# Optimization experiments

Hardware: AMD Instinct MI355X
Metric: run time of the kernel (lower is better)

The kernel has to match this reference:

```python
import jax, jax.numpy as jnp
import numpy as np

BATCH = 2048
OBS_DIM = 48
H0, H1, H2 = 512, 256, 128
ACT_DIM = 12
NUM_TEACHERS = 64


def setup_inputs() -> dict:
    key = jax.random.key(0)
    ks = jax.random.split(key, 10)
    s = lambda fan_in: 1.0 / np.sqrt(fan_in)
    return {
        "obs": jax.random.normal(ks[0], (BATCH, OBS_DIM), dtype=jnp.float32),
        "teacher_indices": jax.random.randint(ks[1], (BATCH,), 0, NUM_TEACHERS),
        "w0": jax.random.normal(ks[2], (NUM_TEACHERS, H0, OBS_DIM), dtype=jnp.float32) * s(OBS_DIM),
        "b0": jax.random.normal(ks[3], (NUM_TEACHERS, H0), dtype=jnp.float32) * s(OBS_DIM),
        "w2": jax.random.normal(ks[4], (NUM_TEACHERS, H1, H0), dtype=jnp.float32) * s(H0),
        "b2": jax.random.normal(ks[5], (NUM_TEACHERS, H1), dtype=jnp.float32) * s(H0),
        "w4": jax.random.normal(ks[6], (NUM_TEACHERS, H2, H1), dtype=jnp.float32) * s(H1),
        "b4": jax.random.normal(ks[7], (NUM_TEACHERS, H2), dtype=jnp.float32) * s(H1),
        "w6": jax.random.normal(ks[8], (NUM_TEACHERS, ACT_DIM, H2), dtype=jnp.float32) * s(H2),
        "b6": jax.random.normal(ks[9], (NUM_TEACHERS, ACT_DIM), dtype=jnp.float32) * s(H2),
    }


def reference(obs, teacher_indices, w0, b0, w2, b2, w4, b4, w6, b6):
    # Per-sample gather of full teacher layer weights, then batched GEMV.
    def layer(x, w, b):
        # x: [B, in]; w[idx]: [B, out, in]; b[idx]: [B, out]
        return jnp.einsum("boi,bi->bo", w[teacher_indices], x) + b[teacher_indices]

    x = jax.nn.elu(layer(obs, w0, b0))
    x = jax.nn.elu(layer(x, w2, b2))
    x = jax.nn.elu(layer(x, w4, b4))
    x = jnp.tanh(layer(x, w6, b6))
    return x
```

## Files before the change

kernel.cpp:

```cpp
#include <hip/hip_runtime.h>

#define BATCH 2048
#define NTEACH 64

typedef __attribute__((ext_vector_type(8))) short short8;
typedef __attribute__((ext_vector_type(4))) float f32x4;

__device__ __forceinline__ unsigned short f2bf(float f) {
    unsigned u = __float_as_uint(f);
    u += 0x7FFFu + ((u >> 16) & 1u);
    return (unsigned short)(u >> 16);
}

__device__ __forceinline__ short8 cvt8(float4 a, float4 b) {
    short8 r;
    r[0] = (short)f2bf(a.x); r[1] = (short)f2bf(a.y);
    r[2] = (short)f2bf(a.z); r[3] = (short)f2bf(a.w);
    r[4] = (short)f2bf(b.x); r[5] = (short)f2bf(b.y);
    r[6] = (short)f2bf(b.z); r[7] = (short)f2bf(b.w);
    return r;
}

__device__ __forceinline__ int2 scan_teacher(const int* __restrict__ tidx,
                                             int t, int* ord) {
    __shared__ int ws_[4];
    const int tid = threadIdx.x;
    const int lane = tid & 63;
    const int wid = tid >> 6;
    int base = 0;
    int my_lt = 0;
#pragma unroll
    for (int r = 0; r < 8; ++r) {
        int i = r * 256 + tid;
        int v = tidx[i];
        bool f = (v == t);
        my_lt += (v < t) ? 1 : 0;
        unsigned long long b = __ballot(f);
        if (lane == 0) ws_[wid] = __builtin_popcountll(b);
        int below = __builtin_popcountll(b & ((1ull << lane) - 1ull));
        __syncthreads();
        int w0 = ws_[0], w1 = ws_[1], w2 = ws_[2], w3 = ws_[3];
        if (ord && f) {
            int wbase = (wid > 0 ? w0 : 0) + (wid > 1 ? w1 : 0) + (wid > 2 ? w2 : 0);
            ord[base + wbase + below] = i;
        }
        base += w0 + w1 + w2 + w3;
        __syncthreads();
    }
    for (int off = 32; off; off >>= 1) my_lt += __shfl_down(my_lt, off);
    if (lane == 0) ws_[wid] = my_lt;
    __syncthreads();
    int start = ws_[0] + ws_[1] + ws_[2] + ws_[3];
    __syncthreads();
    return make_int2(start, base);
}

__global__ __launch_bounds__(256) void l0_kernel(const float* __restrict__ obs,
                                                 const int* __restrict__ tidx,
                                                 const float* __restrict__ w0,
                                                 const float* __restrict__ b0,
                                                 unsigned short* __restrict__ h0) {
    __shared__ int ord[BATCH];
    const int t = blockIdx.y;
    int2 sc = scan_teacher(tidx, t, ord);
    const int start = sc.x, count = sc.y;
    if (count == 0) return;
    const int lane = threadIdx.x & 63, wid = threadIdx.x >> 6;
    const int ln = lane & 15, kg = lane >> 4;
    const int nq = wid & 1, mq = wid >> 1;
    const int n0 = blockIdx.x * 32 + nq * 16;

    short8 bf[2];
    const float* wr = w0 + ((size_t)t * 512 + n0 + ln) * 48;
#pragma unroll
    for (int kt = 0; kt < 2; ++kt) {
        int kb = kt * 32 + kg * 8;
        short8 f8 = {0, 0, 0, 0, 0, 0, 0, 0};
        if (kb < 48) f8 = cvt8(*(const float4*)(wr + kb), *(const float4*)(wr + kb + 4));
        bf[kt] = f8;
    }
    const float bias = b0[(size_t)t * 512 + n0 + ln];

    for (int r0 = mq * 16; r0 < count; r0 += 32) {
        int lr = r0 + ln;
        const float* xr = obs + (size_t)ord[lr < count ? lr : 0] * 48;
        short8 af[2];
#pragma unroll
        for (int kt = 0; kt < 2; ++kt) {
            int kb = kt * 32 + kg * 8;
            short8 f8 = {0, 0, 0, 0, 0, 0, 0, 0};
            if (kb < 48) f8 = cvt8(*(const float4*)(xr + kb), *(const float4*)(xr + kb + 4));
            af[kt] = f8;
        }
        f32x4 acc = {0.f, 0.f, 0.f, 0.f};
        acc = __builtin_amdgcn_mfma_f32_16x16x32_bf16(af[0], bf[0], acc, 0, 0, 0);
        acc = __builtin_amdgcn_mfma_f32_16x16x32_bf16(af[1], bf[1], acc, 0, 0, 0);
#pragma unroll
        for (int j = 0; j < 4; ++j) {
            int row = r0 + kg * 4 + j;
            if (row < count) {
                float v = acc[j] + bias;
                v = v > 0.f ? v : expm1f(v);
                h0[(size_t)(start + row) * 512 + n0 + ln] = f2bf(v);
            }
        }
    }
}

__global__ __launch_bounds__(256) void l1_kernel(const unsigned short* __restrict__ h0,
                                                 const int* __restrict__ tidx,
                                                 const float* __restrict__ w2,
                                                 const float* __restrict__ b2,
                                                 unsigned short* __restrict__ h1) {
    __shared__ f32x4 red[2][64];
    const int t = blockIdx.y;
    int2 sc = scan_teacher(tidx, t, nullptr);
    const int start = sc.x, count = sc.y;
    if (count == 0) return;
    const int lane = threadIdx.x & 63, wid = threadIdx.x >> 6;
    const int ln = lane & 15, kg = lane >> 4;
    const int kq = wid & 1, nq = wid >> 1;
    const int n0 = blockIdx.x * 32 + nq * 16;
    const int kbase = kq * 256;

    short8 bf[8];
    const float* wr = w2 + ((size_t)t * 256 + n0 + ln) * 512 + kbase;
#pragma unroll
    for (int k8 = 0; k8 < 8; ++k8) {
        int kb = k8 * 32 + kg * 8;
        bf[k8] = cvt8(*(const float4*)(wr + kb), *(const float4*)(wr + kb + 4));
    }
    const float bias = b2[(size_t)t * 256 + n0 + ln];

    for (int r0 = 0; r0 < count; r0 += 16) {
        const unsigned short* xr = h0 + (size_t)(start + r0 + ln) * 512 + kbase + kg * 8;
        f32x4 acc = {0.f, 0.f, 0.f, 0.f};
#pragma unroll
        for (int k8 = 0; k8 < 8; ++k8)
            acc = __builtin_amdgcn_mfma_f32_16x16x32_bf16(
                *(const short8*)(xr + k8 * 32), bf[k8], acc, 0, 0, 0);
        __syncthreads();
        if (kq == 1) red[nq][lane] = acc;
        __syncthreads();
        if (kq == 0) {
            f32x4 r = red[nq][lane];
            acc[0] += r[0]; acc[1] += r[1]; acc[2] += r[2]; acc[3] += r[3];
#pragma unroll
            for (int j = 0; j < 4; ++j) {
                int row = r0 + kg * 4 + j;
                if (row < count) {
                    float v = acc[j] + bias;
                    v = v > 0.f ? v : expm1f(v);
                    h1[(size_t)(start + row) * 256 + n0 + ln] = f2bf(v);
                }
            }
        }
    }
}

__global__ __launch_bounds__(256) void l2f_kernel(const unsigned short* __restrict__ h1,
                                                  const int* __restrict__ tidx,
                                                  const float* __restrict__ w4,
                                                  const float* __restrict__ b4,
                                                  const float* __restrict__ w6,
                                                  const float* __restrict__ b6,
                                                  float* __restrict__ out) {
    __shared__ int ord[BATCH];
    __shared__ char h2b[4096];
    const int t = blockIdx.y;
    int2 sc = scan_teacher(tidx, t, ord);
    const int start = sc.x, count = sc.y;
    if ((int)blockIdx.x * 16 >= count) return;
    const int lane = threadIdx.x & 63, wid = threadIdx.x >> 6;
    const int ln = lane & 15, kg = lane >> 4;
    const int nq = wid;

    short8 bfA[2][8];
    float biasA[2];
#pragma unroll
    for (int sub = 0; sub < 2; ++sub) {
        const float* wr = w4 + ((size_t)t * 128 + nq * 32 + sub * 16 + ln) * 256;
#pragma unroll
        for (int k8 = 0; k8 < 8; ++k8) {
            int kb = k8 * 32 + kg * 8;
            bfA[sub][k8] = cvt8(*(const float4*)(wr + kb), *(const float4*)(wr + kb + 4));
        }
        biasA[sub] = b4[(size_t)t * 128 + nq * 32 + sub * 16 + ln];
    }
    short8 bf6[4];
    float bias6 = 0.f;
    if (wid == 0) {
        const float* wr = w6 + ((size_t)t * 12 + (ln < 12 ? ln : 0)) * 128;
#pragma unroll
        for (int kt = 0; kt < 4; ++kt) {
            int kb = kt * 32 + kg * 8;
            bf6[kt] = cvt8(*(const float4*)(wr + kb), *(const float4*)(wr + kb + 4));
        }
        if (ln < 12) bias6 = b6[(size_t)t * 12 + ln];
    }

    for (int mt = blockIdx.x; mt * 16 < count; mt += gridDim.x) {
        const int gr0 = start + mt * 16;
#pragma unroll
        for (int sub = 0; sub < 2; ++sub) {
            const unsigned short* xr = h1 + (size_t)(gr0 + ln) * 256 + kg * 8;
            f32x4 acc = {0.f, 0.f, 0.f, 0.f};
#pragma unroll
            for (int k8 = 0; k8 < 8; ++k8)
                acc = __builtin_amdgcn_mfma_f32_16x16x32_bf16(
                    *(const short8*)(xr + k8 * 32), bfA[sub][k8], acc, 0, 0, 0);
            int col = nq * 32 + sub * 16 + ln;
#pragma unroll
            for (int j = 0; j < 4; ++j) {
                int row = kg * 4 + j;
                float v = acc[j] + biasA[sub];
                v = v > 0.f ? v : expm1f(v);
                int byte = (row * 256 + col * 2) ^ ((row & 7) << 4);
                *(unsigned short*)(h2b + byte) = f2bf(v);
            }
        }
        __syncthreads();
        if (wid == 0) {
            f32x4 acc = {0.f, 0.f, 0.f, 0.f};
#pragma unroll
            for (int kt = 0; kt < 4; ++kt) {
                int byte = (ln * 256 + (kt * 32 + kg * 8) * 2) ^ ((ln & 7) << 4);
                acc = __builtin_amdgcn_mfma_f32_16x16x32_bf16(
                    *(const short8*)(h2b + byte), bf6[kt], acc, 0, 0, 0);
            }
#pragma unroll
            for (int j = 0; j < 4; ++j) {
                int row = mt * 16 + kg * 4 + j;
                if (ln < 12 && row < count)
                    out[(size_t)ord[row] * 12 + ln] = tanhf(acc[j] + bias6);
            }
        }
        __syncthreads();
    }
}

extern "C" void kernel_launch(void* const* d_in, const int* in_sizes, int n_in,
                              void* d_out, int out_size, void* d_ws, size_t ws_size,
                              hipStream_t stream) {
    const float* obs = (const float*)d_in[0];
    const int* tidx  = (const int*)d_in[1];
    const float* w0  = (const float*)d_in[2];
    const float* b0  = (const float*)d_in[3];
    const float* w2  = (const float*)d_in[4];
    const float* b2  = (const float*)d_in[5];
    const float* w4  = (const float*)d_in[6];
    const float* b4  = (const float*)d_in[7];
    const float* w6  = (const float*)d_in[8];
    const float* b6  = (const float*)d_in[9];
    float* out = (float*)d_out;

    const int ROWS = BATCH + 16;
    unsigned short* h0 = (unsigned short*)d_ws;
    unsigned short* h1 = h0 + (size_t)ROWS * 512;

    l0_kernel<<<dim3(16, NTEACH), 256, 0, stream>>>(obs, tidx, w0, b0, h0);
    l1_kernel<<<dim3(8, NTEACH), 256, 0, stream>>>(h0, tidx, w2, b2, h1);
    l2f_kernel<<<dim3(4, NTEACH), 256, 0, stream>>>(h1, tidx, w4, b4, w6, b6, out);
}
```

Baseline: 40.54 us.

## Compute teacher scan once in first layer and share offsets/order via workspace

```diff
diff --git a/kernel.cpp b/kernel.cpp
--- a/kernel.cpp
+++ b/kernel.cpp
@@ -21,65 +21,74 @@
     return r;
 }
 
-__device__ __forceinline__ int2 scan_teacher(const int* __restrict__ tidx,
-                                             int t, int* ord) {
-    __shared__ int ws_[4];
-    const int tid = threadIdx.x;
-    const int lane = tid & 63;
-    const int wid = tid >> 6;
-    int base = 0;
-    int my_lt = 0;
-#pragma unroll
-    for (int r = 0; r < 8; ++r) {
-        int i = r * 256 + tid;
+__device__ __forceinline__ int2 wave_scan(const int* __restrict__ tidx,
+                                          int t, int* ord) {
+    const int lane = threadIdx.x & 63;
+    int base = 0, lt = 0;
+#pragma unroll
+    for (int r = 0; r < 32; ++r) {
+        int i = r * 64 + lane;
         int v = tidx[i];
         bool f = (v == t);
-        my_lt += (v < t) ? 1 : 0;
+        lt += (v < t) ? 1 : 0;
         unsigned long long b = __ballot(f);
-        if (lane == 0) ws_[wid] = __builtin_popcountll(b);
-        int below = __builtin_popcountll(b & ((1ull << lane) - 1ull));
-        __syncthreads();
-        int w0 = ws_[0], w1 = ws_[1], w2 = ws_[2], w3 = ws_[3];
         if (ord && f) {
-            int wbase = (wid > 0 ? w0 : 0) + (wid > 1 ? w1 : 0) + (wid > 2 ? w2 : 0);
-            ord[base + wbase + below] = i;
-        }
-        base += w0 + w1 + w2 + w3;
-        __syncthreads();
-    }
-    for (int off = 32; off; off >>= 1) my_lt += __shfl_down(my_lt, off);
-    if (lane == 0) ws_[wid] = my_lt;
-    __syncthreads();
-    int start = ws_[0] + ws_[1] + ws_[2] + ws_[3];
-    __syncthreads();
-    return make_int2(start, base);
+            int rank = base + __builtin_popcountll(b & ((1ull << lane) - 1ull));
+            ord[rank] = i;
+        }
+        base += __builtin_popcountll(b);
+    }
+#pragma unroll
+    for (int off = 32; off; off >>= 1) lt += __shfl_down(lt, off);
+    lt = __shfl(lt, 0);
+    return make_int2(lt, base);
 }
 
 __global__ __launch_bounds__(256) void l0_kernel(const float* __restrict__ obs,
                                                  const int* __restrict__ tidx,
                                                  const float* __restrict__ w0,
                                                  const float* __restrict__ b0,
+                                                 int* __restrict__ offsets_g,
+                                                 int* __restrict__ order_g,
                                                  unsigned short* __restrict__ h0) {
     __shared__ int ord[BATCH];
     const int t = blockIdx.y;
-    int2 sc = scan_teacher(tidx, t, ord);
-    const int start = sc.x, count = sc.y;
-    if (count == 0) return;
     const int lane = threadIdx.x & 63, wid = threadIdx.x >> 6;
     const int ln = lane & 15, kg = lane >> 4;
     const int nq = wid & 1, mq = wid >> 1;
     const int n0 = blockIdx.x * 32 + nq * 16;
 
-    short8 bf[2];
     const float* wr = w0 + ((size_t)t * 512 + n0 + ln) * 48;
+    bool wvalid[2];
+    float4 wa[2], wb[2];
 #pragma unroll
     for (int kt = 0; kt < 2; ++kt) {
         int kb = kt * 32 + kg * 8;
-        short8 f8 = {0, 0, 0, 0, 0, 0, 0, 0};
-        if (kb < 48) f8 = cvt8(*(const float4*)(wr + kb), *(const float4*)(wr + kb + 4));
-        bf[kt] = f8;
+        wvalid[kt] = kb < 48;
+        const float* p = wr + (wvalid[kt] ? kb : 0);
+        wa[kt] = *(const float4*)p;
+        wb[kt] = *(const float4*)(p + 4);
     }
     const float bias = b0[(size_t)t * 512 + n0 + ln];
+
+    int2 sc = wave_scan(tidx, t, ord);
+    const int start = sc.x, count = sc.y;
+
+    if (blockIdx.x == 0) {
+        if (threadIdx.x == 0) {
+            offsets_g[t] = start;
+            if (t == 0) offsets_g[NTEACH] = BATCH;
+        }
+        for (int i = threadIdx.x; i < count; i += 256) order_g[start + i] = ord[i];
+    }
+    if (count == 0) return;
+
+    short8 bf[2];
+#pragma unroll
+    for (int kt = 0; kt < 2; ++kt) {
+        short8 z = {0, 0, 0, 0, 0, 0, 0, 0};
+        bf[kt] = wvalid[kt] ? cvt8(wa[kt], wb[kt]) : z;
+    }
 
     for (int r0 = mq * 16; r0 < count; r0 += 32) {
         int lr = r0 + ln;
@@ -89,7 +98,8 @@
         for (int kt = 0; kt < 2; ++kt) {
             int kb = kt * 32 + kg * 8;
             short8 f8 = {0, 0, 0, 0, 0, 0, 0, 0};
-            if (kb < 48) f8 = cvt8(*(const float4*)(xr + kb), *(const float4*)(xr + kb + 4));
+            if (kb < 48)
+                f8 = cvt8(*(const float4*)(xr + kb), *(const float4*)(xr + kb + 4));
             af[kt] = f8;
         }
         f32x4 acc = {0.f, 0.f, 0.f, 0.f};
@@ -108,68 +118,66 @@
 }
 
 __global__ __launch_bounds__(256) void l1_kernel(const unsigned short* __restrict__ h0,
-                                                 const int* __restrict__ tidx,
+                                                 const int* __restrict__ offsets_g,
                                                  const float* __restrict__ w2,
                                                  const float* __restrict__ b2,
                                                  unsigned short* __restrict__ h1) {
-    __shared__ f32x4 red[2][64];
     const int t = blockIdx.y;
-    int2 sc = scan_teacher(tidx, t, nullptr);
-    const int start = sc.x, count = sc.y;
+    const int start = offsets_g[t];
+    const int count = offsets_g[t + 1] - start;
     if (count == 0) return;
     const int lane = threadIdx.x & 63, wid = threadIdx.x >> 6;
     const int ln = lane & 15, kg = lane >> 4;
-    const int kq = wid & 1, nq = wid >> 1;
+    const int nq = wid & 1, mq = wid >> 1;
     const int n0 = blockIdx.x * 32 + nq * 16;
-    const int kbase = kq * 256;
-
-    short8 bf[8];
-    const float* wr = w2 + ((size_t)t * 256 + n0 + ln) * 512 + kbase;
-#pragma unroll
-    for (int k8 = 0; k8 < 8; ++k8) {
-        int kb = k8 * 32 + kg * 8;
-        bf[k8] = cvt8(*(const float4*)(wr + kb), *(const float4*)(wr + kb + 4));
-    }
+
+    const float* wr = w2 + ((size_t)t * 256 + n0 + ln) * 512;
     const float bias = b2[(size_t)t * 256 + n0 + ln];
-
-    for (int r0 = 0; r0 < count; r0 += 16) {
-        const unsigned short* xr = h0 + (size_t)(start + r0 + ln) * 512 + kbase + kg * 8;
+    short8 bf[16];
+#pragma unroll
+    for (int g = 0; g < 4; ++g) {
+        float4 ta[4], tb[4];
+#pragma unroll
+        for (int u = 0; u < 4; ++u) {
+            int kb = (g * 4 + u) * 32 + kg * 8;
+            ta[u] = *(const float4*)(wr + kb);
+            tb[u] = *(const float4*)(wr + kb + 4);
+        }
+#pragma unroll
+        for (int u = 0; u < 4; ++u) bf[g * 4 + u] = cvt8(ta[u], tb[u]);
+    }
+
+    for (int r0 = mq * 16; r0 < count; r0 += 32) {
+        const unsigned short* xr = h0 + (size_t)(start + r0 + ln) * 512 + kg * 8;
         f32x4 acc = {0.f, 0.f, 0.f, 0.f};
 #pragma unroll
-        for (int k8 = 0; k8 < 8; ++k8)
+        for (int k8 = 0; k8 < 16; ++k8)
             acc = __builtin_amdgcn_mfma_f32_16x16x32_bf16(
                 *(const short8*)(xr + k8 * 32), bf[k8], acc, 0, 0, 0);
-        __syncthreads();
-        if (kq == 1) red[nq][lane] = acc;
-        __syncthreads();
-        if (kq == 0) {
-            f32x4 r = red[nq][lane];
-            acc[0] += r[0]; acc[1] += r[1]; acc[2] += r[2]; acc[3] += r[3];
-#pragma unroll
-            for (int j = 0; j < 4; ++j) {
-                int row = r0 + kg * 4 + j;
-                if (row < count) {
-                    float v = acc[j] + bias;
-                    v = v > 0.f ? v : expm1f(v);
-                    h1[(size_t)(start + row) * 256 + n0 + ln] = f2bf(v);
-                }
+#pragma unroll
+        for (int j = 0; j < 4; ++j) {
+            int row = r0 + kg * 4 + j;
+            if (row < count) {
+                float v = acc[j] + bias;
+                v = v > 0.f ? v : expm1f(v);
+                h1[(size_t)(start + row) * 256 + n0 + ln] = f2bf(v);
             }
         }
     }
 }
 
 __global__ __launch_bounds__(256) void l2f_kernel(const unsigned short* __restrict__ h1,
-                                                  const int* __restrict__ tidx,
+                                                  const int* __restrict__ offsets_g,
+                                                  const int* __restrict__ order_g,
                                                   const float* __restrict__ w4,
                                                   const float* __restrict__ b4,
                                                   const float* __restrict__ w6,
                                                   const float* __restrict__ b6,
                                                   float* __restrict__ out) {
-    __shared__ int ord[BATCH];
     __shared__ char h2b[4096];
     const int t = blockIdx.y;
-    int2 sc = scan_teacher(tidx, t, ord);
-    const int start = sc.x, count = sc.y;
+    const int start = offsets_g[t];
+    const int count = offsets_g[t + 1] - start;
     if ((int)blockIdx.x * 16 >= count) return;
     const int lane = threadIdx.x & 63, wid = threadIdx.x >> 6;
     const int ln = lane & 15, kg = lane >> 4;
@@ -181,9 +189,16 @@
     for (int sub = 0; sub < 2; ++sub) {
         const float* wr = w4 + ((size_t)t * 128 + nq * 32 + sub * 16 + ln) * 256;
 #pragma unroll
-        for (int k8 = 0; k8 < 8; ++k8) {
-            int kb = k8 * 32 + kg * 8;
-            bfA[sub][k8] = cvt8(*(const float4*)(wr + kb), *(const float4*)(wr + kb + 4));
+        for (int g = 0; g < 2; ++g) {
+            float4 ta[4], tb[4];
+#pragma unroll
+            for (int u = 0; u < 4; ++u) {
+                int kb = (g * 4 + u) * 32 + kg * 8;
+                ta[u] = *(const float4*)(wr + kb);
+                tb[u] = *(const float4*)(wr + kb + 4);
+            }
+#pragma unroll
+            for (int u = 0; u < 4; ++u) bfA[sub][g * 4 + u] = cvt8(ta[u], tb[u]);
         }
         biasA[sub] = b4[(size_t)t * 128 + nq * 32 + sub * 16 + ln];
     }
@@ -232,7 +247,7 @@
             for (int j = 0; j < 4; ++j) {
                 int row = mt * 16 + kg * 4 + j;
                 if (ln < 12 && row < count)
-                    out[(size_t)ord[row] * 12 + ln] = tanhf(acc[j] + bias6);
+                    out[(size_t)order_g[start + row] * 12 + ln] = tanhf(acc[j] + bias6);
             }
         }
         __syncthreads();
@@ -255,10 +270,15 @@
     float* out = (float*)d_out;
 
     const int ROWS = BATCH + 16;
-    unsigned short* h0 = (unsigned short*)d_ws;
+    char* ws = (char*)d_ws;
+    int* offsets = (int*)ws;
+    int* order   = (int*)(ws + 1024);
+    unsigned short* h0 = (unsigned short*)(ws + 16384);
     unsigned short* h1 = h0 + (size_t)ROWS * 512;
 
-    l0_kernel<<<dim3(16, NTEACH), 256, 0, stream>>>(obs, tidx, w0, b0, h0);
-    l1_kernel<<<dim3(8, NTEACH), 256, 0, stream>>>(h0, tidx, w2, b2, h1);
-    l2f_kernel<<<dim3(4, NTEACH), 256, 0, stream>>>(h1, tidx, w4, b4, w6, b6, out);
-}
+    l0_kernel<<<dim3(16, NTEACH), 256, 0, stream>>>(obs, tidx, w0, b0,
+                                                    offsets, order, h0);
+    l1_kernel<<<dim3(8, NTEACH), 256, 0, stream>>>(h0, offsets, w2, b2, h1);
+    l2f_kernel<<<dim3(4, NTEACH), 256, 0, stream>>>(h1, offsets, order,
+                                                    w4, b4, w6, b6, out);
+}
```

Result: slower. 45.54 us (+12.4%).
